# Kernel tuning notes

Measured on AMD Instinct MI355X. Metric: run time of the kernel, lower is better.

Reference implementation:

```python
import jax, jax.numpy as jnp
import numpy as np

FEAT_STRIDE = 16
NMS_THRESH = 0.7
PRE_NMS = 6000   # eval mode: n_test_pre_nms
POST_NMS = 300   # eval mode: n_test_post_nms
MIN_SIZE = 16
NEG = jnp.float32(-1e30)


def _base_anchors(base_size=16, ratios=(0.5, 1.0, 2.0), scales=(8, 16, 32)):
    ctr = (base_size - 1) / 2.0
    size = float(base_size * base_size)
    out = []
    for r in ratios:
        w = np.round(np.sqrt(size / r))
        h = np.round(w * r)
        for s in scales:
            ws, hs = w * s, h * s
            out.append([ctr - 0.5 * (ws - 1), ctr - 0.5 * (hs - 1),
                        ctr + 0.5 * (ws - 1), ctr + 0.5 * (hs - 1)])
    return np.asarray(out, dtype=np.float32)  # (9,4)


def _all_anchors(feat_h, feat_w):
    base = _base_anchors()
    sx = np.arange(feat_w, dtype=np.float32) * FEAT_STRIDE
    sy = np.arange(feat_h, dtype=np.float32) * FEAT_STRIDE
    gx, gy = np.meshgrid(sx, sy)                      # (H,W)
    shifts = np.stack([gx, gy, gx, gy], axis=-1).reshape(-1, 1, 4)
    anchors = (shifts + base[None, :, :]).reshape(-1, 4)  # (H*W*9,4), order (h,w,a)
    return jnp.asarray(anchors)


def _nms_keep(boxes):
    # boxes sorted by descending score; torchvision IoU convention (no +1)
    n = boxes.shape[0]
    area = (boxes[:, 2] - boxes[:, 0]) * (boxes[:, 3] - boxes[:, 1])
    lt = jnp.maximum(boxes[:, None, :2], boxes[None, :, :2])  # (N,N,2)
    rb = jnp.minimum(boxes[:, None, 2:], boxes[None, :, 2:])
    wh = jnp.clip(rb - lt, 0.0)
    inter = wh[..., 0] * wh[..., 1]
    iou = inter / (area[:, None] + area[None, :] - inter)
    over = iou > NMS_THRESH
    idx = jnp.arange(n)

    def body(i, supp):
        row = over[i] & (idx > i) & jnp.logical_not(supp[i])
        return supp | row

    supp = jax.lax.fori_loop(0, n, body, jnp.zeros((n,), bool))
    keep = jnp.nonzero(~supp, size=POST_NMS, fill_value=0)[0]
    return keep


def reference(rpn_cls_scores, rpn_bbox_preds, img_h, img_w):
    feat_h, feat_w = rpn_cls_scores.shape[2], rpn_cls_scores.shape[3]
    anchors = _all_anchors(feat_h, feat_w)                      # (K,4)
    scores = jax.nn.softmax(
        rpn_cls_scores.transpose(0, 2, 3, 1).reshape(-1, 2), axis=1)[:, 1]
    deltas = rpn_bbox_preds.transpose(0, 2, 3, 1).reshape(-1, 4)

    widths = anchors[:, 2] - anchors[:, 0] + 1.0
    heights = anchors[:, 3] - anchors[:, 1] + 1.0
    ctr_x = anchors[:, 0] + 0.5 * widths
    ctr_y = anchors[:, 1] + 0.5 * heights
    dx, dy, dw, dh = deltas[:, 0], deltas[:, 1], deltas[:, 2], deltas[:, 3]
    pcx = dx * widths + ctr_x
    pcy = dy * heights + ctr_y
    pw = jnp.exp(dw) * widths
    ph = jnp.exp(dh) * heights

    x1 = jnp.clip(pcx - 0.5 * pw, 0.0, img_w - 1)
    y1 = jnp.clip(pcy - 0.5 * ph, 0.0, img_h - 1)
    x2 = jnp.clip(pcx + 0.5 * pw, 0.0, img_w - 1)
    y2 = jnp.clip(pcy + 0.5 * ph, 0.0, img_h - 1)
    proposals = jnp.stack([x1, y1, x2, y2], axis=1)             # (K,4)

    valid = ((x2 - x1 + 1.0) >= MIN_SIZE) & ((y2 - y1 + 1.0) >= MIN_SIZE)
    masked = jnp.where(valid, scores, NEG)
    _, order = jax.lax.top_k(masked, PRE_NMS)                   # sort desc + pre-nms cut
    boxes = proposals[order]                                    # (PRE_NMS,4)

    keep = _nms_keep(boxes)
    kept = boxes[keep]                                          # (POST_NMS,4)
    batch_inds = jnp.zeros((POST_NMS, 1), dtype=kept.dtype)
    return jnp.concatenate([batch_inds, kept], axis=1)          # (POST_NMS,5)


def setup_inputs() -> dict:
    key = jax.random.key(0)
    k1, k2 = jax.random.split(key)
    rpn_cls_scores = jax.random.normal(k1, (1, 18, 64, 100), dtype=jnp.float32)
    rpn_bbox_preds = 0.2 * jax.random.normal(k2, (1, 36, 64, 100), dtype=jnp.float32)
    return {"rpn_cls_scores": rpn_cls_scores, "rpn_bbox_preds": rpn_bbox_preds,
            "img_h": 1024, "img_w": 1600}
```

## Files before the change

kernel.cpp:

```cpp
#include <hip/hip_runtime.h>

typedef unsigned long long u64;
typedef unsigned int u32;

#define FEAT_W 100
#define NANCH 9
#define NTOT 57600
#define NPAD 65536
#define PRE_NMS 6000
#define POST_NMS 300
#define NBLK 94
#define NCHUNK 24
#define CH_STRIDE 6400
#define CHUNK 1024

__constant__ double c_base[9][4] = {
    {-84.0, -40.0, 99.0, 55.0},    {-176.0, -88.0, 191.0, 103.0},
    {-360.0, -184.0, 375.0, 199.0},{-56.0, -56.0, 71.0, 71.0},
    {-120.0, -120.0, 135.0, 135.0},{-248.0, -248.0, 263.0, 263.0},
    {-36.0, -80.0, 51.0, 95.0},    {-80.0, -168.0, 95.0, 183.0},
    {-168.0, -344.0, 183.0, 359.0}};

struct BoxD { double x1, y1, x2, y2; };

__device__ __forceinline__ int packed_off(int i) {
  int q = i >> 6, r = i & 63;
  return 94 * i - 32 * q * (q - 1) - r * q;
}

__device__ __forceinline__ BoxD decode_box(int i, const float* __restrict__ bbox,
                                           double imw1, double imh1) {
  int pos = i / NANCH;
  int a = i - pos * NANCH;
  int h = pos / FEAT_W;
  int w = pos - h * FEAT_W;
  double ax1 = c_base[a][0] + 16.0 * (double)w;
  double ay1 = c_base[a][1] + 16.0 * (double)h;
  double ax2 = c_base[a][2] + 16.0 * (double)w;
  double ay2 = c_base[a][3] + 16.0 * (double)h;
  double wd = ax2 - ax1 + 1.0;
  double hg = ay2 - ay1 + 1.0;
  double cx = ax1 + 0.5 * wd;
  double cy = ay1 + 0.5 * hg;
  const float* bp = bbox + (size_t)(4 * a) * CH_STRIDE + pos;
  double dx = (double)bp[0];
  double dy = (double)bp[CH_STRIDE];
  double dw = (double)bp[2 * CH_STRIDE];
  double dh = (double)bp[3 * CH_STRIDE];
  double pcx = dx * wd + cx;
  double pcy = dy * hg + cy;
  double pw = exp(dw) * wd;
  double ph = exp(dh) * hg;
  BoxD b;
  b.x1 = fmin(fmax(pcx - 0.5 * pw, 0.0), imw1);
  b.y1 = fmin(fmax(pcy - 0.5 * ph, 0.0), imh1);
  b.x2 = fmin(fmax(pcx + 0.5 * pw, 0.0), imw1);
  b.y2 = fmin(fmax(pcy + 0.5 * ph, 0.0), imh1);
  return b;
}

__device__ __forceinline__ u64 score_key(int i, const float* __restrict__ cls,
                                         const float* __restrict__ bbox,
                                         double imw1, double imh1) {
  BoxD b = decode_box(i, bbox, imw1, imh1);
  bool valid = (b.x2 - b.x1 + 1.0 >= 16.0) && (b.y2 - b.y1 + 1.0 >= 16.0);
  int pos = i / NANCH;
  int a = i - pos * NANCH;
  double c0 = (double)cls[(size_t)(2 * a) * CH_STRIDE + pos];
  double c1 = (double)cls[(size_t)(2 * a + 1) * CH_STRIDE + pos];
  double masked = valid ? (c1 - c0) : -1e30;
  u64 u = (u64)__double_as_longlong(masked);
  return (u >> 63) ? ~u : (u | 0x8000000000000000ULL);
}

__device__ __forceinline__ bool before(u64 ka, u32 va, u64 kb, u32 vb) {
  return (ka > kb) || (ka == kb && va < vb);
}
__device__ __forceinline__ bool comes_after(u64 ka, u32 va, u64 kb, u32 vb) {
  return (ka < kb) || (ka == kb && va > vb);
}

__global__ __launch_bounds__(512) void k_score_sort(
    const float* __restrict__ cls, const float* __restrict__ bbox,
    const int* __restrict__ imh, const int* __restrict__ imw,
    u64* __restrict__ keys, u32* __restrict__ vals) {
  __shared__ u64 sk[CHUNK];
  __shared__ u32 sv[CHUNK];
  int base = blockIdx.x * CHUNK;
  double imh1 = (double)(imh[0] - 1);
  double imw1 = (double)(imw[0] - 1);
  for (int t = threadIdx.x; t < CHUNK; t += 512) {
    int i = base + t;
    if (i < NTOT) { sk[t] = score_key(i, cls, bbox, imw1, imh1); sv[t] = (u32)i; }
    else { sk[t] = 0ULL; sv[t] = (u32)i; }
  }
  __syncthreads();
  bool prev_cross = false;
  for (int k = 2; k <= CHUNK; k <<= 1) {
    for (int j = k >> 1; j > 0; j >>= 1) {
      bool cross = (j >= 128);
      if (cross || prev_cross) __syncthreads();
      int t = threadIdx.x;
      int i = ((t & ~(j - 1)) << 1) | (t & (j - 1));
      int l = i | j;
      bool up = ((i & k) == 0);
      u64 ka = sk[i], kb = sk[l];
      u32 va = sv[i], vb = sv[l];
      if (comes_after(ka, va, kb, vb) == up) { sk[i] = kb; sv[i] = vb; sk[l] = ka; sv[l] = va; }
      prev_cross = cross;
    }
  }
  __syncthreads();
  for (int t = threadIdx.x; t < CHUNK; t += 512) { keys[base + t] = sk[t]; vals[base + t] = sv[t]; }
}

template <int N, int STEPS>
__device__ __forceinline__ int rank7(
    const u64* __restrict__ K0, const u32* __restrict__ V0,
    const u64* __restrict__ K1, const u32* __restrict__ V1,
    const u64* __restrict__ K2, const u32* __restrict__ V2,
    const u64* __restrict__ K3, const u32* __restrict__ V3,
    const u64* __restrict__ K4, const u32* __restrict__ V4,
    const u64* __restrict__ K5, const u32* __restrict__ V5,
    const u64* __restrict__ K6, const u32* __restrict__ V6,
    u64 k, u32 v) {
  int lo0 = 0, hi0 = N, lo1 = 0, hi1 = N, lo2 = 0, hi2 = N;
  int lo3 = 0, hi3 = N, lo4 = 0, hi4 = N, lo5 = 0, hi5 = N;
  int lo6 = 0, hi6 = N;
  #pragma unroll
  for (int st = 0; st < STEPS; ++st) {
    int m0 = (lo0 + hi0) >> 1, m1 = (lo1 + hi1) >> 1, m2 = (lo2 + hi2) >> 1;
    int m3 = (lo3 + hi3) >> 1, m4 = (lo4 + hi4) >> 1, m5 = (lo5 + hi5) >> 1;
    int m6 = (lo6 + hi6) >> 1;
    int c0 = min(m0, N - 1), c1 = min(m1, N - 1), c2 = min(m2, N - 1);
    int c3 = min(m3, N - 1), c4 = min(m4, N - 1), c5 = min(m5, N - 1);
    int c6 = min(m6, N - 1);
    u64 k0 = K0[c0], k1 = K1[c1], k2 = K2[c2], k3 = K3[c3];
    u64 k4 = K4[c4], k5 = K5[c5], k6 = K6[c6];
    u32 v0 = V0[c0], v1 = V1[c1], v2 = V2[c2], v3 = V3[c3];
    u32 v4 = V4[c4], v5 = V5[c5], v6 = V6[c6];
    if (lo0 < hi0) { if (before(k0, v0, k, v)) lo0 = m0 + 1; else hi0 = m0; }
    if (lo1 < hi1) { if (before(k1, v1, k, v)) lo1 = m1 + 1; else hi1 = m1; }
    if (lo2 < hi2) { if (before(k2, v2, k, v)) lo2 = m2 + 1; else hi2 = m2; }
    if (lo3 < hi3) { if (before(k3, v3, k, v)) lo3 = m3 + 1; else hi3 = m3; }
    if (lo4 < hi4) { if (before(k4, v4, k, v)) lo4 = m4 + 1; else hi4 = m4; }
    if (lo5 < hi5) { if (before(k5, v5, k, v)) lo5 = m5 + 1; else hi5 = m5; }
    if (lo6 < hi6) { if (before(k6, v6, k, v)) lo6 = m6 + 1; else hi6 = m6; }
  }
  return lo0 + lo1 + lo2 + lo3 + lo4 + lo5 + lo6;
}

__global__ void k_merge1(const u64* __restrict__ Ak, const u32* __restrict__ Av,
                         u64* __restrict__ Bk, u32* __restrict__ Bv) {
  int gtid = blockIdx.x * blockDim.x + threadIdx.x;
  if (gtid >= NPAD) return;
  int lst = gtid >> 10, pos = gtid & 1023, grp = lst >> 3;
  u64 k = Ak[gtid]; u32 v = Av[gtid];
  int b0 = grp << 3, q = lst & 7;
  int i0 = 0 + (0 >= q), i1 = 1 + (1 >= q), i2 = 2 + (2 >= q);
  int i3 = 3 + (3 >= q), i4 = 4 + (4 >= q), i5 = 5 + (5 >= q);
  int i6 = 6 + (6 >= q);
  int rank = pos + rank7<1024, 11>(
      Ak + (size_t)(b0 + i0) * 1024, Av + (size_t)(b0 + i0) * 1024,
      Ak + (size_t)(b0 + i1) * 1024, Av + (size_t)(b0 + i1) * 1024,
      Ak + (size_t)(b0 + i2) * 1024, Av + (size_t)(b0 + i2) * 1024,
      Ak + (size_t)(b0 + i3) * 1024, Av + (size_t)(b0 + i3) * 1024,
      Ak + (size_t)(b0 + i4) * 1024, Av + (size_t)(b0 + i4) * 1024,
      Ak + (size_t)(b0 + i5) * 1024, Av + (size_t)(b0 + i5) * 1024,
      Ak + (size_t)(b0 + i6) * 1024, Av + (size_t)(b0 + i6) * 1024, k, v);
  Bk[(size_t)grp * 8192 + rank] = k;
  Bv[(size_t)grp * 8192 + rank] = v;
}

__global__ void k_merge2(const u64* __restrict__ Bk, const u32* __restrict__ Bv,
                         const float* __restrict__ bbox, const int* __restrict__ imh,
                         const int* __restrict__ imw, float4* __restrict__ fboxes) {
  int gtid = blockIdx.x * blockDim.x + threadIdx.x;
  if (gtid >= NPAD) return;
  int lst = gtid >> 13, pos = gtid & 8191;
  u64 k = Bk[gtid]; u32 v = Bv[gtid];
  int i0 = 0 + (0 >= lst), i1 = 1 + (1 >= lst), i2 = 2 + (2 >= lst);
  int i3 = 3 + (3 >= lst), i4 = 4 + (4 >= lst), i5 = 5 + (5 >= lst);
  int i6 = 6 + (6 >= lst);
  int rank = pos + rank7<8192, 14>(
      Bk + (size_t)i0 * 8192, Bv + (size_t)i0 * 8192,
      Bk + (size_t)i1 * 8192, Bv + (size_t)i1 * 8192,
      Bk + (size_t)i2 * 8192, Bv + (size_t)i2 * 8192,
      Bk + (size_t)i3 * 8192, Bv + (size_t)i3 * 8192,
      Bk + (size_t)i4 * 8192, Bv + (size_t)i4 * 8192,
      Bk + (size_t)i5 * 8192, Bv + (size_t)i5 * 8192,
      Bk + (size_t)i6 * 8192, Bv + (size_t)i6 * 8192, k, v);
  if (rank < PRE_NMS) {
    double imh1 = (double)(imh[0] - 1);
    double imw1 = (double)(imw[0] - 1);
    BoxD b = decode_box((int)v, bbox, imw1, imh1);
    fboxes[rank] = make_float4((float)b.x1, (float)b.y1, (float)b.x2, (float)b.y2);
  }
}

__global__ void k_mask(const float4* __restrict__ fboxes, u64* __restrict__ mask,
                       u64* __restrict__ colC) {
  __shared__ float4 cb[64];
  int bc = blockIdx.x, br = blockIdx.y;
  int t = threadIdx.x;
  bool samechunk = (bc >> 2) == (br >> 2);
  if (bc < br) {
    if (samechunk) colC[(size_t)(((bc << 6) + t) * 4 + (br & 3))] = 0;
    return;
  }
  int j0 = bc * 64;
  int jt = j0 + t;
  cb[t] = (jt < PRE_NMS) ? fboxes[jt] : make_float4(0.f, 0.f, 0.f, 0.f);
  __syncthreads();
  int i = br * 64 + t;
  u64 bits = 0;
  if (i < PRE_NMS) {
    float4 rb = fboxes[i];
    float areai = (rb.z - rb.x) * (rb.w - rb.y);
    int cmax = min(64, PRE_NMS - j0);
    for (int c = 0; c < cmax; ++c) {
      int j = j0 + c;
      if (j <= i) continue;
      float4 cbx = cb[c];
      float xx1 = fmaxf(rb.x, cbx.x), yy1 = fmaxf(rb.y, cbx.y);
      float xx2 = fminf(rb.z, cbx.z), yy2 = fminf(rb.w, cbx.w);
      float w = fmaxf(xx2 - xx1, 0.0f), h = fmaxf(yy2 - yy1, 0.0f);
      float inter = w * h;
      float areaj = (cbx.z - cbx.x) * (cbx.w - cbx.y);
      float iou = inter / (areai + areaj - inter);
      if (iou > 0.7f) bits |= (1ULL << c);
    }
    mask[(size_t)(packed_off(i) + (bc - br))] = bits;
  }
  if (samechunk) {
    u64 colbits = 0;
    for (int j2 = 0; j2 < 64; ++j2) {
      u64 bl = __ballot(((bits >> j2) & 1ULL) != 0);
      if (t == j2) colbits = bl;
    }
    colC[(size_t)(((bc << 6) + t) * 4 + (br & 3))] = colbits;
  }
}

__device__ __forceinline__ u64 valid_word(int w) {
  int base = w << 6;
  if (base >= PRE_NMS) return 0ULL;
  if (base + 64 <= PRE_NMS) return ~0ULL;
  return (1ULL << (PRE_NMS - base)) - 1ULL;
}

__global__ __launch_bounds__(64) void k_scan(const u64* __restrict__ mask,
                                             const u64* __restrict__ colC,
                                             const float4* __restrict__ fboxes,
                                             float* __restrict__ out) {
  __shared__ int keepIdx[384];
  __shared__ int keepA[384];
  int lane = threadIdx.x;
  for (int r = lane; r < 384; r += 64) { keepIdx[r] = 0; keepA[r] = 0; }
  int nkeep = 0;
  bool done = false;
  int a0 = 0, a1 = 0, a2 = 0, a3 = 0, a4 = 0;
  u64 or0 = 0, or1 = 0, or2 = 0, or3 = 0;

  u64 ct00, ct01, ct02, ct03, ct10, ct11, ct12, ct13;
  u64 ct20, ct21, ct22, ct23, ct30, ct31, ct32, ct33;

#define COL_LOAD(cc, T, x0, x1, x2, x3)                                        \
  {                                                                            \
    int J_ = ((cc) << 8) + ((T) << 6) + lane;                                  \
    x0 = 0; x1 = 0; x2 = 0; x3 = 0;                                            \
    if (J_ < PRE_NMS) {                                                        \
      const ulonglong2* p_ = (const ulonglong2*)(colC + (size_t)J_ * 4);       \
      ulonglong2 u_ = p_[0], w_ = p_[1];                                       \
      x0 = u_.x; x1 = u_.y; x2 = w_.x; x3 = w_.y;                              \
    }                                                                          \
  }

  COL_LOAD(0, 0, ct00, ct01, ct02, ct03)
  COL_LOAD(0, 1, ct10, ct11, ct12, ct13)
  COL_LOAD(0, 2, ct20, ct21, ct22, ct23)
  COL_LOAD(0, 3, ct30, ct31, ct32, ct33)

  for (int c = 0; c < NCHUNK && !done; ++c) {
    int wbase = c << 2;
    int wnext = wbase + 4;
    bool gnext = (c + 1 < NCHUNK);
    bool tail_n = (wnext + 2) < NBLK;
    int oldn = nkeep;

    u64 n00 = 0, n01 = 0, n02 = 0, n03 = 0, n10 = 0, n11 = 0, n12 = 0, n13 = 0;
    u64 n20 = 0, n21 = 0, n22 = 0, n23 = 0, n30 = 0, n31 = 0, n32 = 0, n33 = 0;
    if (gnext) {
      COL_LOAD(c + 1, 0, n00, n01, n02, n03)
      COL_LOAD(c + 1, 1, n10, n11, n12, n13)
      COL_LOAD(c + 1, 2, n20, n21, n22, n23)
      COL_LOAD(c + 1, 3, n30, n31, n32, n33)
    }

    u64 e0 = 0, e1 = 0, e2 = 0, e3 = 0;
    if (gnext) {
#define EGATHER(AA, LIM)                                                       \
      if ((LIM) < oldn) {                                                      \
        const u64* p_ = mask + (size_t)(AA) + wnext;                           \
        e0 |= p_[0]; e1 |= p_[1];                                              \
        if (tail_n) { e2 |= p_[2]; e3 |= p_[3]; }                              \
      }
      EGATHER(a0, lane)
      EGATHER(a1, 64 + lane)
      EGATHER(a2, 128 + lane)
      EGATHER(a3, 192 + lane)
      EGATHER(a4, 256 + lane)
#undef EGATHER
    }

    u64 kf0 = 0, kf1 = 0, kf2 = 0, kf3 = 0;

#define RUN_WORD(OR_, TT, DIAGC, CROSS_EXPR, KFVAR)                            \
    if (!done) {                                                               \
      u64 alive = ~(OR_) & valid_word(wbase + (TT));                           \
      alive &= ~__ballot((CROSS_EXPR) != 0ULL);                                \
      u64 kfacc = 0;                                                           \
      while (alive) {                                                          \
        int b = __builtin_ctzll(alive);                                        \
        u64 bb = 1ULL << b;                                                    \
        kfacc |= bb;                                                           \
        u64 sup_ = __ballot((((DIAGC) >> b) & 1ULL) != 0ULL);                  \
        alive &= ~(sup_ | bb);                                                 \
      }                                                                        \
      KFVAR = kfacc;                                                           \
      if (kfacc) {                                                             \
        if ((kfacc >> lane) & 1ULL) {                                          \
          int idx = nkeep + __popcll(kfacc & ((1ULL << lane) - 1ULL));         \
          if (idx < 384) {                                                     \
            int K = (c << 8) + ((TT) << 6) + lane;                             \
            keepIdx[idx] = K;                                                  \
            keepA[idx] = packed_off(K) - (K >> 6);                             \
          }                                                                    \
        }                                                                      \
        nkeep += __popcll(kfacc);                                              \
        if (nkeep >= POST_NMS) done = true;                                    \
      }                                                                        \
    }

    RUN_WORD(or0, 0, ct00, 0ULL, kf0)
    RUN_WORD(or1, 1, ct11, (ct10 & kf0), kf1)
    RUN_WORD(or2, 2, ct22, (ct20 & kf0) | (ct21 & kf1), kf2)
    RUN_WORD(or3, 3, ct33, (ct30 & kf0) | (ct31 & kf1) | (ct32 & kf2), kf3)
#undef RUN_WORD
    (void)kf3;

    if (gnext && !done) {
      int nk = min(nkeep, 384);
#define LGATHER(AR, SLOT)                                                      \
      {                                                                        \
        int s_ = (SLOT);                                                       \
        if (s_ >= oldn && s_ < nk) {                                           \
          AR = keepA[s_];                                                      \
          const u64* p_ = mask + (size_t)AR + wnext;                           \
          e0 |= p_[0]; e1 |= p_[1];                                            \
          if (tail_n) { e2 |= p_[2]; e3 |= p_[3]; }                            \
        }                                                                      \
      }
      LGATHER(a0, lane)
      LGATHER(a1, 64 + lane)
      LGATHER(a2, 128 + lane)
      LGATHER(a3, 192 + lane)
      LGATHER(a4, 256 + lane)
#undef LGATHER
      #pragma unroll
      for (int m = 32; m; m >>= 1) {
        e0 |= __shfl_xor(e0, m);
        e1 |= __shfl_xor(e1, m);
        e2 |= __shfl_xor(e2, m);
        e3 |= __shfl_xor(e3, m);
      }
      or0 = e0; or1 = e1; or2 = e2; or3 = e3;
    }

    ct00 = n00; ct01 = n01; ct02 = n02; ct03 = n03;
    ct10 = n10; ct11 = n11; ct12 = n12; ct13 = n13;
    ct20 = n20; ct21 = n21; ct22 = n22; ct23 = n23;
    ct30 = n30; ct31 = n31; ct32 = n32; ct33 = n33;
  }
#undef COL_LOAD
  __syncthreads();

  for (int r = lane; r < POST_NMS; r += 64) {
    int kk = keepIdx[r];
    float4 b = fboxes[kk];
    float* o = out + r * 5;
    o[0] = 0.0f;
    o[1] = b.x;
    o[2] = b.y;
    o[3] = b.z;
    o[4] = b.w;
  }
}

extern "C" void kernel_launch(void* const* d_in, const int* in_sizes, int n_in,
                              void* d_out, int out_size, void* d_ws, size_t ws_size,
                              hipStream_t stream) {
  const float* cls = (const float*)d_in[0];
  const float* bbox = (const float*)d_in[1];
  const int* imh = (const int*)d_in[2];
  const int* imw = (const int*)d_in[3];
  float* out = (float*)d_out;

  char* p = (char*)d_ws;
  float4* fboxes = (float4*)p;
  u64* colC = (u64*)(p + 96256);
  char* mb = p + 385024;
  u64* maskbuf = (u64*)mb;
  u64* Ak = (u64*)mb;
  u32* Av = (u32*)(mb + 524288);
  u64* Bk = (u64*)(mb + 786432);
  u32* Bv = (u32*)(mb + 1310720);

  k_score_sort<<<64, 512, 0, stream>>>(cls, bbox, imh, imw, Ak, Av);
  k_merge1<<<NPAD / 256, 256, 0, stream>>>(Ak, Av, Bk, Bv);
  k_merge2<<<NPAD / 256, 256, 0, stream>>>(Bk, Bv, bbox, imh, imw, fboxes);
  k_mask<<<dim3(NBLK, NBLK), 64, 0, stream>>>(fboxes, maskbuf, colC);
  k_scan<<<1, 64, 0, stream>>>(maskbuf, colC, fboxes, out);
}
```

Before: 151.6 us.

## Pipeline NMS scan by deferring previous-chunk suppression to column masks

The mask kernel now also stores, for each column, transposed suppression bits from the previous 256-box chunk, which doubles colC to 8 words per box. The serial scan uses these bits together with the previous chunk's keep flags to apply suppression from the immediately preceding chunk. The gather of mask words for newly kept boxes therefore moves off the critical path and lags by one chunk, with the shuffle reduction done at the start of the next iteration. In exchange the scan carries more registers and loads twice as much column data, and the mask kernel does extra ballot work for adjacent-chunk blocks.

Result: no change. 151.0 us (-0.4%).

```diff
diff --git a/kernel.cpp b/kernel.cpp
--- a/kernel.cpp
+++ b/kernel.cpp
@@ -203,9 +203,11 @@
   __shared__ float4 cb[64];
   int bc = blockIdx.x, br = blockIdx.y;
   int t = threadIdx.x;
+  int J = (bc << 6) + t;
   bool samechunk = (bc >> 2) == (br >> 2);
+  bool prevchunk = (bc >> 2) == (br >> 2) + 1;
   if (bc < br) {
-    if (samechunk) colC[(size_t)(((bc << 6) + t) * 4 + (br & 3))] = 0;
+    if (samechunk) colC[(size_t)J * 8 + 4 + (br & 3)] = 0;
     return;
   }
   int j0 = bc * 64;
@@ -232,13 +234,19 @@
     }
     mask[(size_t)(packed_off(i) + (bc - br))] = bits;
   }
-  if (samechunk) {
+  if (samechunk || prevchunk) {
     u64 colbits = 0;
     for (int j2 = 0; j2 < 64; ++j2) {
       u64 bl = __ballot(((bits >> j2) & 1ULL) != 0);
       if (t == j2) colbits = bl;
     }
-    colC[(size_t)(((bc << 6) + t) * 4 + (br & 3))] = colbits;
+    colC[(size_t)J * 8 + (samechunk ? 4 : 0) + (br & 3)] = colbits;
+  }
+  if (bc == br && bc < 4) {
+    colC[(size_t)J * 8 + 0] = 0;
+    colC[(size_t)J * 8 + 1] = 0;
+    colC[(size_t)J * 8 + 2] = 0;
+    colC[(size_t)J * 8 + 3] = 0;
   }
 }
 
@@ -259,27 +267,30 @@
   for (int r = lane; r < 384; r += 64) { keepIdx[r] = 0; keepA[r] = 0; }
   int nkeep = 0;
   bool done = false;
-  int a0 = 0, a1 = 0, a2 = 0, a3 = 0, a4 = 0;
-  u64 or0 = 0, or1 = 0, or2 = 0, or3 = 0;
-
-  u64 ct00, ct01, ct02, ct03, ct10, ct11, ct12, ct13;
-  u64 ct20, ct21, ct22, ct23, ct30, ct31, ct32, ct33;
-
-#define COL_LOAD(cc, T, x0, x1, x2, x3)                                        \
+  u64 e0 = 0, e1 = 0, e2 = 0, e3 = 0;
+  u64 kfp0 = 0, kfp1 = 0, kfp2 = 0, kfp3 = 0;
+
+  u64 pt00, pt01, pt02, pt03, ct00, ct01, ct02, ct03;
+  u64 pt10, pt11, pt12, pt13, ct10, ct11, ct12, ct13;
+  u64 pt20, pt21, pt22, pt23, ct20, ct21, ct22, ct23;
+  u64 pt30, pt31, pt32, pt33, ct30, ct31, ct32, ct33;
+
+#define COL_LOAD8(cc, X, p0, p1, p2, p3, t0, t1, t2, t3)                       \
   {                                                                            \
-    int J_ = ((cc) << 8) + ((T) << 6) + lane;                                  \
-    x0 = 0; x1 = 0; x2 = 0; x3 = 0;                                            \
+    int J_ = ((cc) << 8) + ((X) << 6) + lane;                                  \
+    p0 = 0; p1 = 0; p2 = 0; p3 = 0; t0 = 0; t1 = 0; t2 = 0; t3 = 0;            \
     if (J_ < PRE_NMS) {                                                        \
-      const ulonglong2* p_ = (const ulonglong2*)(colC + (size_t)J_ * 4);       \
-      ulonglong2 u_ = p_[0], w_ = p_[1];                                       \
-      x0 = u_.x; x1 = u_.y; x2 = w_.x; x3 = w_.y;                              \
+      const ulonglong2* q_ = (const ulonglong2*)(colC + (size_t)J_ * 8);       \
+      ulonglong2 A_ = q_[0], B_ = q_[1], C_ = q_[2], D_ = q_[3];               \
+      p0 = A_.x; p1 = A_.y; p2 = B_.x; p3 = B_.y;                              \
+      t0 = C_.x; t1 = C_.y; t2 = D_.x; t3 = D_.y;                              \
     }                                                                          \
   }
 
-  COL_LOAD(0, 0, ct00, ct01, ct02, ct03)
-  COL_LOAD(0, 1, ct10, ct11, ct12, ct13)
-  COL_LOAD(0, 2, ct20, ct21, ct22, ct23)
-  COL_LOAD(0, 3, ct30, ct31, ct32, ct33)
+  COL_LOAD8(0, 0, pt00, pt01, pt02, pt03, ct00, ct01, ct02, ct03)
+  COL_LOAD8(0, 1, pt10, pt11, pt12, pt13, ct10, ct11, ct12, ct13)
+  COL_LOAD8(0, 2, pt20, pt21, pt22, pt23, ct20, ct21, ct22, ct23)
+  COL_LOAD8(0, 3, pt30, pt31, pt32, pt33, ct30, ct31, ct32, ct33)
 
   for (int c = 0; c < NCHUNK && !done; ++c) {
     int wbase = c << 2;
@@ -288,28 +299,40 @@
     bool tail_n = (wnext + 2) < NBLK;
     int oldn = nkeep;
 
-    u64 n00 = 0, n01 = 0, n02 = 0, n03 = 0, n10 = 0, n11 = 0, n12 = 0, n13 = 0;
-    u64 n20 = 0, n21 = 0, n22 = 0, n23 = 0, n30 = 0, n31 = 0, n32 = 0, n33 = 0;
+    u64 or0 = e0, or1 = e1, or2 = e2, or3 = e3;
+    #pragma unroll
+    for (int m = 32; m; m >>= 1) {
+      or0 |= __shfl_xor(or0, m);
+      or1 |= __shfl_xor(or1, m);
+      or2 |= __shfl_xor(or2, m);
+      or3 |= __shfl_xor(or3, m);
+    }
+
+    u64 np00 = 0, np01 = 0, np02 = 0, np03 = 0, nt00 = 0, nt01 = 0, nt02 = 0, nt03 = 0;
+    u64 np10 = 0, np11 = 0, np12 = 0, np13 = 0, nt10 = 0, nt11 = 0, nt12 = 0, nt13 = 0;
+    u64 np20 = 0, np21 = 0, np22 = 0, np23 = 0, nt20 = 0, nt21 = 0, nt22 = 0, nt23 = 0;
+    u64 np30 = 0, np31 = 0, np32 = 0, np33 = 0, nt30 = 0, nt31 = 0, nt32 = 0, nt33 = 0;
     if (gnext) {
-      COL_LOAD(c + 1, 0, n00, n01, n02, n03)
-      COL_LOAD(c + 1, 1, n10, n11, n12, n13)
-      COL_LOAD(c + 1, 2, n20, n21, n22, n23)
-      COL_LOAD(c + 1, 3, n30, n31, n32, n33)
-    }
-
-    u64 e0 = 0, e1 = 0, e2 = 0, e3 = 0;
+      COL_LOAD8(c + 1, 0, np00, np01, np02, np03, nt00, nt01, nt02, nt03)
+      COL_LOAD8(c + 1, 1, np10, np11, np12, np13, nt10, nt11, nt12, nt13)
+      COL_LOAD8(c + 1, 2, np20, np21, np22, np23, nt20, nt21, nt22, nt23)
+      COL_LOAD8(c + 1, 3, np30, np31, np32, np33, nt30, nt31, nt32, nt33)
+    }
+
+    e0 = 0; e1 = 0; e2 = 0; e3 = 0;
     if (gnext) {
-#define EGATHER(AA, LIM)                                                       \
-      if ((LIM) < oldn) {                                                      \
-        const u64* p_ = mask + (size_t)(AA) + wnext;                           \
+#define EGATHER(SLOT)                                                          \
+      if ((SLOT) < oldn) {                                                     \
+        int aa_ = keepA[SLOT];                                                 \
+        const u64* p_ = mask + (size_t)aa_ + wnext;                            \
         e0 |= p_[0]; e1 |= p_[1];                                              \
         if (tail_n) { e2 |= p_[2]; e3 |= p_[3]; }                              \
       }
-      EGATHER(a0, lane)
-      EGATHER(a1, 64 + lane)
-      EGATHER(a2, 128 + lane)
-      EGATHER(a3, 192 + lane)
-      EGATHER(a4, 256 + lane)
+      EGATHER(lane)
+      EGATHER(64 + lane)
+      EGATHER(128 + lane)
+      EGATHER(192 + lane)
+      EGATHER(256 + lane)
 #undef EGATHER
     }
 
@@ -342,47 +365,30 @@
       }                                                                        \
     }
 
-    RUN_WORD(or0, 0, ct00, 0ULL, kf0)
-    RUN_WORD(or1, 1, ct11, (ct10 & kf0), kf1)
-    RUN_WORD(or2, 2, ct22, (ct20 & kf0) | (ct21 & kf1), kf2)
-    RUN_WORD(or3, 3, ct33, (ct30 & kf0) | (ct31 & kf1) | (ct32 & kf2), kf3)
+    RUN_WORD(or0, 0, ct00,
+             (pt00 & kfp0) | (pt01 & kfp1) | (pt02 & kfp2) | (pt03 & kfp3), kf0)
+    RUN_WORD(or1, 1, ct11,
+             (pt10 & kfp0) | (pt11 & kfp1) | (pt12 & kfp2) | (pt13 & kfp3) |
+             (ct10 & kf0), kf1)
+    RUN_WORD(or2, 2, ct22,
+             (pt20 & kfp0) | (pt21 & kfp1) | (pt22 & kfp2) | (pt23 & kfp3) |
+             (ct20 & kf0) | (ct21 & kf1), kf2)
+    RUN_WORD(or3, 3, ct33,
+             (pt30 & kfp0) | (pt31 & kfp1) | (pt32 & kfp2) | (pt33 & kfp3) |
+             (ct30 & kf0) | (ct31 & kf1) | (ct32 & kf2), kf3)
 #undef RUN_WORD
-    (void)kf3;
-
-    if (gnext && !done) {
-      int nk = min(nkeep, 384);
-#define LGATHER(AR, SLOT)                                                      \
-      {                                                                        \
-        int s_ = (SLOT);                                                       \
-        if (s_ >= oldn && s_ < nk) {                                           \
-          AR = keepA[s_];                                                      \
-          const u64* p_ = mask + (size_t)AR + wnext;                           \
-          e0 |= p_[0]; e1 |= p_[1];                                            \
-          if (tail_n) { e2 |= p_[2]; e3 |= p_[3]; }                            \
-        }                                                                      \
-      }
-      LGATHER(a0, lane)
-      LGATHER(a1, 64 + lane)
-      LGATHER(a2, 128 + lane)
-      LGATHER(a3, 192 + lane)
-      LGATHER(a4, 256 + lane)
-#undef LGATHER
-      #pragma unroll
-      for (int m = 32; m; m >>= 1) {
-        e0 |= __shfl_xor(e0, m);
-        e1 |= __shfl_xor(e1, m);
-        e2 |= __shfl_xor(e2, m);
-        e3 |= __shfl_xor(e3, m);
-      }
-      or0 = e0; or1 = e1; or2 = e2; or3 = e3;
-    }
-
-    ct00 = n00; ct01 = n01; ct02 = n02; ct03 = n03;
-    ct10 = n10; ct11 = n11; ct12 = n12; ct13 = n13;
-    ct20 = n20; ct21 = n21; ct22 = n22; ct23 = n23;
-    ct30 = n30; ct31 = n31; ct32 = n32; ct33 = n33;
-  }
-#undef COL_LOAD
+
+    kfp0 = kf0; kfp1 = kf1; kfp2 = kf2; kfp3 = kf3;
+    pt00 = np00; pt01 = np01; pt02 = np02; pt03 = np03;
+    pt10 = np10; pt11 = np11; pt12 = np12; pt13 = np13;
+    pt20 = np20; pt21 = np21; pt22 = np22; pt23 = np23;
+    pt30 = np30; pt31 = np31; pt32 = np32; pt33 = np33;
+    ct00 = nt00; ct01 = nt01; ct02 = nt02; ct03 = nt03;
+    ct10 = nt10; ct11 = nt11; ct12 = nt12; ct13 = nt13;
+    ct20 = nt20; ct21 = nt21; ct22 = nt22; ct23 = nt23;
+    ct30 = nt30; ct31 = nt31; ct32 = nt32; ct33 = nt33;
+  }
+#undef COL_LOAD8
   __syncthreads();
 
   for (int r = lane; r < POST_NMS; r += 64) {
@@ -409,7 +415,7 @@
   char* p = (char*)d_ws;
   float4* fboxes = (float4*)p;
   u64* colC = (u64*)(p + 96256);
-  char* mb = p + 385024;
+  char* mb = p + 481280;
   u64* maskbuf = (u64*)mb;
   u64* Ak = (u64*)mb;
   u32* Av = (u32*)(mb + 524288);
```
